# Kernel optimization log

Hardware: AMD Instinct MI355X
Metric: run time of the kernel (lower is better)

## Reference

```python
import jax, jax.numpy as jnp
import numpy as np

MARGIN = 1.0
EPS = 1e-6  # torch.nn.PairwiseDistance default eps (added to the difference vector)


def setup_inputs() -> dict:
    key = jax.random.key(0)
    k1, k2 = jax.random.split(key)
    B, D = 8192, 256
    out = jax.random.normal(k1, (B, D), dtype=jnp.float32)
    label = jax.random.randint(k2, (B,), 0, 2, dtype=jnp.int64)
    return {"out": out, "label": label}


def reference(out, label):
    B, D = out.shape
    # PairwiseDistance: dist_ij = || out_i - out_j + eps ||_2
    # Expand: sum_k (d_k + eps)^2 = ||d||^2 + 2*eps*sum_k d_k + D*eps^2
    sq_norm = jnp.sum(out * out, axis=-1)                       # [B]
    gram = out @ out.T                                          # [B, B]
    sq = sq_norm[:, None] + sq_norm[None, :] - 2.0 * gram       # ||out_i - out_j||^2
    row_sum = jnp.sum(out, axis=-1)                             # [B]
    sq_eps = sq + 2.0 * EPS * (row_sum[:, None] - row_sum[None, :]) + D * EPS * EPS
    dist = jnp.sqrt(jnp.maximum(sq_eps, 1e-12))                 # [B, B]

    same = label[:, None] == label[None, :]                     # [B, B] bool
    pos = dist * dist
    neg = jnp.square(jnp.maximum(MARGIN - dist, 0.0))
    per_pair = jnp.where(same, pos, neg)

    # only i < j pairs (strict upper triangle)
    tri = jnp.triu(jnp.ones((B, B), dtype=out.dtype), k=1)
    loss = jnp.sum(per_pair * tri)
    cnt = B * (B - 1) // 2
    return loss / (cnt + 1e-6)
```

## Files before the change

### kernel.cpp

```cpp
#include <hip/hip_runtime.h>
#include <hip/hip_fp8.h>

#define B_ 8192
#define D_ 256
#define KS_ 64
#define EPS_ 1e-6f
#define MARGIN_ 1.0f
#define NT_ 64
#define NTILES_ (NT_ * (NT_ + 1) / 2)
#define CEPS_ ((float)D_ * EPS_ * EPS_)
#define SCREEN_ 17.0f

typedef float floatx4 __attribute__((ext_vector_type(4)));

#define XBF_BYTES (B_ * D_ * 2)
#define OFF_P    0
#define OFF_Q    8192
#define OFF_S0   16384
#define OFF_S1   16640
#define OFF_N0   16896
#define OFF_N1   16897
#define OFF_C0   16898
#define OFF_ACC  16899
#define ZERO_OFF 16384
#define ZERO_CNT 516

__device__ __forceinline__ int trif(int t) { return (t * (129 - t)) / 2; }
__device__ __forceinline__ int decode_ti(int t) {
    int ti = (int)((129.0f - sqrtf(fmaxf(16641.0f - 8.0f * (float)t, 0.0f))) * 0.5f);
    ti = max(0, min(63, ti));
    while (trif(ti + 1) <= t) ++ti;
    while (trif(ti) > t) --ti;
    return ti;
}

__device__ __noinline__ float exact_hinge(const float* __restrict__ x, int gi, int gj,
                                          const int* __restrict__ label) {
    if (label[gi] == label[gj]) return 0.0f;
    const float* xi = x + (size_t)gi * D_;
    const float* xj = x + (size_t)gj * D_;
    float sq = 0.0f;
    for (int k = 0; k < D_; ++k) {
        const float df = xi[k] - xj[k] + EPS_;
        sq += df * df;
    }
    if (sq < 1.0f) {
        const float d = sqrtf(fmaxf(sq, 1e-12f));
        const float h = MARGIN_ - d;
        return h * h;
    }
    return 0.0f;
}

__global__ __launch_bounds__(256) void prep_kernel(
    const float* __restrict__ x, const int* __restrict__ label,
    unsigned char* __restrict__ xqT, float* __restrict__ fws) {
    float* pS = fws + OFF_P;   float* qS = fws + OFF_Q;

    __shared__ int lab_s[32];
    __shared__ float spn[32];
    __shared__ float colbuf0[4][256], colbuf1[4][256];

    const int blk = blockIdx.x;
    const int r0 = blk * 32;
    const int tid = threadIdx.x, w = tid >> 6, lane = tid & 63;

    if (tid < 32) lab_s[tid] = label[r0 + tid];
    __syncthreads();

    floatx4 t0 = (floatx4)0.0f, t1 = (floatx4)0.0f;
    #pragma unroll
    for (int i = 0; i < 8; ++i) {
        const int rloc = w * 8 + i;
        const int row = r0 + rloc;
        const floatx4 v = *(const floatx4*)(x + (size_t)row * D_ + lane * 4);
        float sq = v[0]*v[0] + v[1]*v[1] + v[2]*v[2] + v[3]*v[3];
        float rs = v[0] + v[1] + v[2] + v[3];
        #pragma unroll
        for (int off = 8; off; off >>= 1) {
            sq += __shfl_down(sq, off);
            rs += __shfl_down(rs, off);
        }
        const float sqS = sq, rsS = rs;
        sq += __shfl_down(sq, 16); rs += __shfl_down(rs, 16);
        sq += __shfl_down(sq, 32); rs += __shfl_down(rs, 32);
        if (lane == 0) {
            pS[row] = sqS + 2.0f * EPS_ * rsS;
            qS[row] = sqS - 2.0f * EPS_ * rsS;
            spn[rloc] = sq;
        }
        if (lab_s[rloc]) t1 += v; else t0 += v;
        if (lane < 16) {
            __hip_fp8_e4m3 c0(v[0]), c1(v[1]), c2(v[2]), c3(v[3]);
            const unsigned int u = (unsigned int)c0.__x | ((unsigned int)c1.__x << 8)
                                 | ((unsigned int)c2.__x << 16) | ((unsigned int)c3.__x << 24);
            const int R = row >> 4, r = row & 15;
            const int ks = lane >> 3, quad = (lane >> 1) & 3, b = (lane & 1) * 4;
            *(unsigned int*)(xqT + (((R * 2 + ks) << 9) | (quad << 7) | (r << 3) | b)) = u;
        }
    }
    *(floatx4*)&colbuf0[w][lane * 4] = t0;
    *(floatx4*)&colbuf1[w][lane * 4] = t1;
    __syncthreads();

    atomicAdd(fws + OFF_S0 + tid,
              colbuf0[0][tid] + colbuf0[1][tid] + colbuf0[2][tid] + colbuf0[3][tid]);
    atomicAdd(fws + OFF_S1 + tid,
              colbuf1[0][tid] + colbuf1[1][tid] + colbuf1[2][tid] + colbuf1[3][tid]);

    if (tid < 32) {
        const float n = spn[tid];
        const int lb = lab_s[tid];
        float n0 = lb ? 0.0f : n, n1 = lb ? n : 0.0f;
        float c0 = lb ? 0.0f : 1.0f;
        #pragma unroll
        for (int off = 16; off; off >>= 1) {
            n0 += __shfl_down(n0, off);
            n1 += __shfl_down(n1, off);
            c0 += __shfl_down(c0, off);
        }
        if (tid == 0) {
            atomicAdd(fws + OFF_N0, n0);
            atomicAdd(fws + OFF_N1, n1);
            atomicAdd(fws + OFF_C0, c0);
        }
    }
}

__global__ __launch_bounds__(256, 3) void detect_kernel(
    const unsigned char* __restrict__ xqT, const float* __restrict__ x,
    const int* __restrict__ label, float* __restrict__ fws) {
    const float* pS = fws + OFF_P;  const float* qS = fws + OFF_Q;
    float* acc = fws + OFF_ACC;

    const int ti = decode_ti(blockIdx.x);
    const int tj = ti + (blockIdx.x - trif(ti));
    const int i0 = ti * 128, j0 = tj * 128;

    const int tid = threadIdx.x, wave = tid >> 6, lane = tid & 63;
    const int quad = lane >> 4, r = lane & 15;
    const int wm = wave >> 1, wn = wave & 1;

    const int Ri = (i0 >> 4) + wm * 4;
    const int Rj = (j0 >> 4) + wn * 4;
    const int lo = (quad << 7) | (r << 3);
    long av[8], bv[8];
    #pragma unroll
    for (int mt = 0; mt < 4; ++mt)
        #pragma unroll
        for (int ks = 0; ks < 2; ++ks) {
            av[mt * 2 + ks] = *(const long*)(xqT + ((((Ri + mt) * 2 + ks) << 9) | lo));
            bv[mt * 2 + ks] = *(const long*)(xqT + ((((Rj + mt) * 2 + ks) << 9) | lo));
        }

    floatx4 accv[16];
    #pragma unroll
    for (int t = 0; t < 16; ++t) accv[t] = (floatx4)0.0f;

    #pragma unroll
    for (int ks = 0; ks < 2; ++ks)
        #pragma unroll
        for (int mt = 0; mt < 4; ++mt)
            #pragma unroll
            for (int nt = 0; nt < 4; ++nt)
                accv[mt * 4 + nt] = __builtin_amdgcn_mfma_f32_16x16x32_fp8_fp8(
                    av[mt * 2 + ks], bv[nt * 2 + ks], accv[mt * 4 + nt], 0, 0, 0);

    float s = 0.0f;
    if (ti != tj) {
        float m = -1e30f;
        #pragma unroll
        for (int t = 0; t < 16; ++t)
            m = fmaxf(m, fmaxf(fmaxf(accv[t][0], accv[t][1]), fmaxf(accv[t][2], accv[t][3])));
        float pv = pS[i0 + wm * 64 + lane];
        float qv = qS[j0 + wn * 64 + lane];
        #pragma unroll
        for (int off = 32; off; off >>= 1) {
            pv = fminf(pv, __shfl_down(pv, off));
            qv = fminf(qv, __shfl_down(qv, off));
        }
        const float pmn = __shfl(pv, 0), qmn = __shfl(qv, 0);
        if (__any(2.0f * m > pmn + qmn - SCREEN_)) {
            #pragma unroll
            for (int mt = 0; mt < 4; ++mt)
                #pragma unroll
                for (int nt = 0; nt < 4; ++nt)
                    #pragma unroll
                    for (int reg = 0; reg < 4; ++reg) {
                        const int gi = i0 + wm * 64 + mt * 16 + quad * 4 + reg;
                        const int gj = j0 + wn * 64 + nt * 16 + r;
                        const float sq8 = pS[gi] + qS[gj] - 2.0f * accv[mt * 4 + nt][reg];
                        if (sq8 < SCREEN_) s += exact_hinge(x, gi, gj, label);
                    }
        }
    } else {
        #pragma unroll
        for (int mt = 0; mt < 4; ++mt)
            #pragma unroll
            for (int nt = 0; nt < 4; ++nt)
                #pragma unroll
                for (int reg = 0; reg < 4; ++reg) {
                    const int il = wm * 64 + mt * 16 + quad * 4 + reg;
                    const int jl = wn * 64 + nt * 16 + r;
                    if (il < jl) {
                        const int gi = i0 + il, gj = j0 + jl;
                        const float sq8 = pS[gi] + qS[gj] - 2.0f * accv[mt * 4 + nt][reg];
                        if (sq8 < SCREEN_) s += exact_hinge(x, gi, gj, label);
                    }
                }
    }
    #pragma unroll
    for (int off = 32; off; off >>= 1) s += __shfl_down(s, off);
    if (lane == 0 && s != 0.0f) atomicAdd(acc, s);
}

__global__ __launch_bounds__(256) void finalize_kernel(
    const float* __restrict__ fws, float* __restrict__ out) {
    __shared__ float red[4];
    const int tid = threadIdx.x, w = tid >> 6, lane = tid & 63;

    const float a = fws[OFF_S0 + tid], b = fws[OFF_S1 + tid];
    float v = a * a + b * b;
    #pragma unroll
    for (int off = 32; off; off >>= 1) v += __shfl_down(v, off);
    if (lane == 0) red[w] = v;
    __syncthreads();

    if (tid == 0) {
        const double Tsq = (double)red[0] + (double)red[1] + (double)red[2] + (double)red[3];
        const double N0 = fws[OFF_N0], N1 = fws[OFF_N1];
        const double C0 = fws[OFF_C0], C1 = (double)B_ - C0;
        const double same = C0 * N0 + C1 * N1 - Tsq
                          + 0.5 * (C0 * (C0 - 1.0) + C1 * (C1 - 1.0)) * (double)CEPS_;
        const double total = same + (double)fws[OFF_ACC];
        const double cnt = (double)B_ * (double)(B_ - 1) / 2.0 + 1e-6;
        out[0] = (float)(total / cnt);
    }
}

extern "C" void kernel_launch(void* const* d_in, const int* in_sizes, int n_in,
                              void* d_out, int out_size, void* d_ws, size_t ws_size,
                              hipStream_t stream) {
    const float* x = (const float*)d_in[0];
    const int* label = (const int*)d_in[1];
    float* out = (float*)d_out;

    char* ws = (char*)d_ws;
    unsigned char* xqT = (unsigned char*)ws;
    float* fws = (float*)(ws + XBF_BYTES);

    hipMemsetAsync(fws + ZERO_OFF, 0, ZERO_CNT * sizeof(float), stream);
    prep_kernel<<<B_ / 32, 256, 0, stream>>>(x, label, xqT, fws);
    detect_kernel<<<NTILES_, 256, 0, stream>>>(xqT, x, label, fws);
    finalize_kernel<<<1, 256, 0, stream>>>(fws, out);
}
```

Measured before the change: 94.35 us.

## Fuse finalize into detect via last-block counter and use persistent 768-block grid

The separate finalize kernel is removed. The last detect block to finish, found through an atomic done counter, now computes the final loss, which saves one launch and its gap. The detect grid drops from 2080 tiles to 768 blocks that each loop over up to 3 tiles, which cuts block scheduling overhead and the number of partial-sum atomics. In exchange, load balance gets coarser, and the reduction now depends on threadfence and atomic ordering to be correct.

```diff
diff --git a/kernel.cpp b/kernel.cpp
--- a/kernel.cpp
+++ b/kernel.cpp
@@ -8,6 +8,7 @@
 #define MARGIN_ 1.0f
 #define NT_ 64
 #define NTILES_ (NT_ * (NT_ + 1) / 2)
+#define GRID_ 768
 #define CEPS_ ((float)D_ * EPS_ * EPS_)
 #define SCREEN_ 17.0f
 
@@ -22,8 +23,9 @@
 #define OFF_N1   16897
 #define OFF_C0   16898
 #define OFF_ACC  16899
+#define OFF_DONE 16900
 #define ZERO_OFF 16384
-#define ZERO_CNT 516
+#define ZERO_CNT 517
 
 __device__ __forceinline__ int trif(int t) { return (t * (129 - t)) / 2; }
 __device__ __forceinline__ int decode_ti(int t) {
@@ -129,112 +131,131 @@
 
 __global__ __launch_bounds__(256, 3) void detect_kernel(
     const unsigned char* __restrict__ xqT, const float* __restrict__ x,
-    const int* __restrict__ label, float* __restrict__ fws) {
+    const int* __restrict__ label, float* __restrict__ fws,
+    float* __restrict__ out) {
     const float* pS = fws + OFF_P;  const float* qS = fws + OFF_Q;
     float* acc = fws + OFF_ACC;
-
-    const int ti = decode_ti(blockIdx.x);
-    const int tj = ti + (blockIdx.x - trif(ti));
-    const int i0 = ti * 128, j0 = tj * 128;
+    unsigned* done = (unsigned*)(fws + OFF_DONE);
 
     const int tid = threadIdx.x, wave = tid >> 6, lane = tid & 63;
     const int quad = lane >> 4, r = lane & 15;
     const int wm = wave >> 1, wn = wave & 1;
-
-    const int Ri = (i0 >> 4) + wm * 4;
-    const int Rj = (j0 >> 4) + wn * 4;
     const int lo = (quad << 7) | (r << 3);
-    long av[8], bv[8];
-    #pragma unroll
-    for (int mt = 0; mt < 4; ++mt)
-        #pragma unroll
-        for (int ks = 0; ks < 2; ++ks) {
-            av[mt * 2 + ks] = *(const long*)(xqT + ((((Ri + mt) * 2 + ks) << 9) | lo));
-            bv[mt * 2 + ks] = *(const long*)(xqT + ((((Rj + mt) * 2 + ks) << 9) | lo));
-        }
-
-    floatx4 accv[16];
-    #pragma unroll
-    for (int t = 0; t < 16; ++t) accv[t] = (floatx4)0.0f;
-
-    #pragma unroll
-    for (int ks = 0; ks < 2; ++ks)
+
+    __shared__ float red[4];
+    __shared__ int last_s;
+
+    float s = 0.0f;
+
+    #pragma unroll 1
+    for (int tt = 0; tt < 3; ++tt) {
+        const int t = blockIdx.x + tt * GRID_;
+        if (t >= NTILES_) break;
+        const int ti = decode_ti(t);
+        const int tj = ti + (t - trif(ti));
+        const int i0 = ti * 128, j0 = tj * 128;
+
+        const int Ri = (i0 >> 4) + wm * 4;
+        const int Rj = (j0 >> 4) + wn * 4;
+        long av[8], bv[8];
         #pragma unroll
         for (int mt = 0; mt < 4; ++mt)
             #pragma unroll
-            for (int nt = 0; nt < 4; ++nt)
-                accv[mt * 4 + nt] = __builtin_amdgcn_mfma_f32_16x16x32_fp8_fp8(
-                    av[mt * 2 + ks], bv[nt * 2 + ks], accv[mt * 4 + nt], 0, 0, 0);
-
-    float s = 0.0f;
-    if (ti != tj) {
-        float m = -1e30f;
-        #pragma unroll
-        for (int t = 0; t < 16; ++t)
-            m = fmaxf(m, fmaxf(fmaxf(accv[t][0], accv[t][1]), fmaxf(accv[t][2], accv[t][3])));
-        float pv = pS[i0 + wm * 64 + lane];
-        float qv = qS[j0 + wn * 64 + lane];
-        #pragma unroll
-        for (int off = 32; off; off >>= 1) {
-            pv = fminf(pv, __shfl_down(pv, off));
-            qv = fminf(qv, __shfl_down(qv, off));
-        }
-        const float pmn = __shfl(pv, 0), qmn = __shfl(qv, 0);
-        if (__any(2.0f * m > pmn + qmn - SCREEN_)) {
+            for (int ks = 0; ks < 2; ++ks) {
+                av[mt * 2 + ks] = *(const long*)(xqT + ((((Ri + mt) * 2 + ks) << 9) | lo));
+                bv[mt * 2 + ks] = *(const long*)(xqT + ((((Rj + mt) * 2 + ks) << 9) | lo));
+            }
+
+        floatx4 accv[16];
+        #pragma unroll
+        for (int t2 = 0; t2 < 16; ++t2) accv[t2] = (floatx4)0.0f;
+
+        #pragma unroll
+        for (int ks = 0; ks < 2; ++ks)
+            #pragma unroll
+            for (int mt = 0; mt < 4; ++mt)
+                #pragma unroll
+                for (int nt = 0; nt < 4; ++nt)
+                    accv[mt * 4 + nt] = __builtin_amdgcn_mfma_f32_16x16x32_fp8_fp8(
+                        av[mt * 2 + ks], bv[nt * 2 + ks], accv[mt * 4 + nt], 0, 0, 0);
+
+        if (ti != tj) {
+            float m = -1e30f;
+            #pragma unroll
+            for (int t2 = 0; t2 < 16; ++t2)
+                m = fmaxf(m, fmaxf(fmaxf(accv[t2][0], accv[t2][1]),
+                                   fmaxf(accv[t2][2], accv[t2][3])));
+            float pv = pS[i0 + wm * 64 + lane];
+            float qv = qS[j0 + wn * 64 + lane];
+            #pragma unroll
+            for (int off = 32; off; off >>= 1) {
+                pv = fminf(pv, __shfl_down(pv, off));
+                qv = fminf(qv, __shfl_down(qv, off));
+            }
+            const float pmn = __shfl(pv, 0), qmn = __shfl(qv, 0);
+            if (__any(2.0f * m > pmn + qmn - SCREEN_)) {
+                #pragma unroll
+                for (int mt = 0; mt < 4; ++mt)
+                    #pragma unroll
+                    for (int nt = 0; nt < 4; ++nt)
+                        #pragma unroll
+                        for (int reg = 0; reg < 4; ++reg) {
+                            const int gi = i0 + wm * 64 + mt * 16 + quad * 4 + reg;
+                            const int gj = j0 + wn * 64 + nt * 16 + r;
+                            const float sq8 = pS[gi] + qS[gj] - 2.0f * accv[mt * 4 + nt][reg];
+                            if (sq8 < SCREEN_) s += exact_hinge(x, gi, gj, label);
+                        }
+            }
+        } else {
             #pragma unroll
             for (int mt = 0; mt < 4; ++mt)
                 #pragma unroll
                 for (int nt = 0; nt < 4; ++nt)
                     #pragma unroll
                     for (int reg = 0; reg < 4; ++reg) {
-                        const int gi = i0 + wm * 64 + mt * 16 + quad * 4 + reg;
-                        const int gj = j0 + wn * 64 + nt * 16 + r;
-                        const float sq8 = pS[gi] + qS[gj] - 2.0f * accv[mt * 4 + nt][reg];
-                        if (sq8 < SCREEN_) s += exact_hinge(x, gi, gj, label);
+                        const int il = wm * 64 + mt * 16 + quad * 4 + reg;
+                        const int jl = wn * 64 + nt * 16 + r;
+                        if (il < jl) {
+                            const int gi = i0 + il, gj = j0 + jl;
+                            const float sq8 = pS[gi] + qS[gj] - 2.0f * accv[mt * 4 + nt][reg];
+                            if (sq8 < SCREEN_) s += exact_hinge(x, gi, gj, label);
+                        }
                     }
         }
-    } else {
-        #pragma unroll
-        for (int mt = 0; mt < 4; ++mt)
-            #pragma unroll
-            for (int nt = 0; nt < 4; ++nt)
-                #pragma unroll
-                for (int reg = 0; reg < 4; ++reg) {
-                    const int il = wm * 64 + mt * 16 + quad * 4 + reg;
-                    const int jl = wn * 64 + nt * 16 + r;
-                    if (il < jl) {
-                        const int gi = i0 + il, gj = j0 + jl;
-                        const float sq8 = pS[gi] + qS[gj] - 2.0f * accv[mt * 4 + nt][reg];
-                        if (sq8 < SCREEN_) s += exact_hinge(x, gi, gj, label);
-                    }
-                }
-    }
+    }
+
     #pragma unroll
     for (int off = 32; off; off >>= 1) s += __shfl_down(s, off);
     if (lane == 0 && s != 0.0f) atomicAdd(acc, s);
-}
-
-__global__ __launch_bounds__(256) void finalize_kernel(
-    const float* __restrict__ fws, float* __restrict__ out) {
-    __shared__ float red[4];
-    const int tid = threadIdx.x, w = tid >> 6, lane = tid & 63;
-
-    const float a = fws[OFF_S0 + tid], b = fws[OFF_S1 + tid];
-    float v = a * a + b * b;
-    #pragma unroll
-    for (int off = 32; off; off >>= 1) v += __shfl_down(v, off);
-    if (lane == 0) red[w] = v;
-    __syncthreads();
-
+
+    __syncthreads();
     if (tid == 0) {
-        const double Tsq = (double)red[0] + (double)red[1] + (double)red[2] + (double)red[3];
-        const double N0 = fws[OFF_N0], N1 = fws[OFF_N1];
-        const double C0 = fws[OFF_C0], C1 = (double)B_ - C0;
-        const double same = C0 * N0 + C1 * N1 - Tsq
-                          + 0.5 * (C0 * (C0 - 1.0) + C1 * (C1 - 1.0)) * (double)CEPS_;
-        const double total = same + (double)fws[OFF_ACC];
-        const double cnt = (double)B_ * (double)(B_ - 1) / 2.0 + 1e-6;
-        out[0] = (float)(total / cnt);
+        __threadfence();
+        last_s = (atomicAdd(done, 1u) == GRID_ - 1u);
+    }
+    __syncthreads();
+    if (!last_s) return;
+
+    {
+        const float a = fws[OFF_S0 + tid], b = fws[OFF_S1 + tid];
+        float v = a * a + b * b;
+        #pragma unroll
+        for (int off = 32; off; off >>= 1) v += __shfl_down(v, off);
+        if (lane == 0) red[wave] = v;
+        __syncthreads();
+
+        if (tid == 0) {
+            const double Tsq = (double)red[0] + (double)red[1]
+                             + (double)red[2] + (double)red[3];
+            const double N0 = fws[OFF_N0], N1 = fws[OFF_N1];
+            const double C0 = fws[OFF_C0], C1 = (double)B_ - C0;
+            const double same = C0 * N0 + C1 * N1 - Tsq
+                              + 0.5 * (C0 * (C0 - 1.0) + C1 * (C1 - 1.0)) * (double)CEPS_;
+            const double hinge = (double)atomicAdd(acc, 0.0f);
+            const double total = same + hinge;
+            const double cnt = (double)B_ * (double)(B_ - 1) / 2.0 + 1e-6;
+            out[0] = (float)(total / cnt);
+        }
     }
 }
 
@@ -251,6 +272,5 @@
 
     hipMemsetAsync(fws + ZERO_OFF, 0, ZERO_CNT * sizeof(float), stream);
     prep_kernel<<<B_ / 32, 256, 0, stream>>>(x, label, xqT, fws);
-    detect_kernel<<<NTILES_, 256, 0, stream>>>(xqT, x, label, fws);
-    finalize_kernel<<<1, 256, 0, stream>>>(fws, out);
-}
+    detect_kernel<<<GRID_, 256, 0, stream>>>(xqT, x, label, fws, out);
+}
```

Measured after the change: 103.1 us. 9.2% more time.
